# Optimization experiments

Measured on AMD Instinct MI355X. Metric: run time of the kernel, lower is better.

Reference implementation:

```python
import jax, jax.numpy as jnp
import numpy as np

B, S, D_MODEL = 8, 2048, 512
G, V = 2, 320          # num_groups, num_vars
CV_DIM = 256 // G      # proj_dim // num_groups = 128
TAU = 2.0


def setup_inputs() -> dict:
    key = jax.random.key(0)
    k1, k2, k3, k4, k5 = jax.random.split(key, 5)
    hidden_states = jax.random.normal(k1, (B, S, D_MODEL), dtype=jnp.float32)
    # Linear(d_model -> G*V); store as (in, out) for direct matmul
    W = jax.random.normal(k2, (D_MODEL, G * V), dtype=jnp.float32) * (1.0 / np.sqrt(D_MODEL))
    b = jax.random.normal(k3, (G * V,), dtype=jnp.float32) * 0.01
    codevectors = jax.random.normal(k4, (1, G * V, CV_DIM), dtype=jnp.float32)
    # pre-sampled Gumbel(0,1) noise, shape (B*S*G, V)
    u = jax.random.uniform(k5, (B * S * G, V), dtype=jnp.float32,
                           minval=1e-10, maxval=1.0)
    gumbels = -jnp.log(-jnp.log(u))
    return {"hidden_states": hidden_states, "W": W, "b": b,
            "codevectors": codevectors, "gumbels": gumbels}


def reference(hidden_states, W, b, codevectors, gumbels):
    Bs, Ss, _ = hidden_states.shape
    N = Bs * Ss
    # weight projection: (B,S,D) @ (D,G*V) -> (B,S,G*V)
    logits = hidden_states @ W + b
    logits = logits.reshape(N * G, V).astype(jnp.float32)

    # gumbel-softmax, hard=True with straight-through
    y_soft = jax.nn.softmax((logits + gumbels) / TAU, axis=-1)  # (N*G, V)
    idx = jnp.argmax(y_soft, axis=-1)
    y_hard = jax.nn.one_hot(idx, V, dtype=y_soft.dtype)
    codevector_probs = y_hard - jax.lax.stop_gradient(y_soft) + y_soft

    # perplexity from the (noise-free) soft distribution
    soft_dist = jax.nn.softmax(logits.reshape(N, G, V), axis=-1)
    marginal = soft_dist.mean(axis=0)                            # (G, V)
    perplexity = jnp.exp(-jnp.sum(marginal * jnp.log(marginal + 1e-7),
                                  axis=-1)).sum()

    # codebook lookup as weighted sum (equivalent to one-hot gather)
    cv = codevectors.reshape(G, V, CV_DIM)
    probs = codevector_probs.reshape(N, G, V)
    out = jnp.einsum('ngv,gvd->ngd', probs, cv)                  # (N, G, d)
    out = out.reshape(Bs, Ss, G * CV_DIM)
    return out, perplexity
```

## Files before the change

kernel.cpp:

```cpp
#include <hip/hip_runtime.h>

#define M_ROWS 16384
#define K_DIM  512
#define N_COLS 640
#define V_CODES 320
#define CV_DIM 128

typedef _Float16 half8 __attribute__((ext_vector_type(8)));
typedef _Float16 half4v __attribute__((ext_vector_type(4)));
typedef float floatx4 __attribute__((ext_vector_type(4)));

__device__ inline void gll16(const void* g, void* l) {
    __builtin_amdgcn_global_load_lds(
        (const __attribute__((address_space(1))) void*)g,
        (__attribute__((address_space(3))) void*)l, 16, 0, 0);
}

__global__ __launch_bounds__(256)
void prepW(const float* __restrict__ W, _Float16* __restrict__ Wt,
           float* __restrict__ marginal) {
    __shared__ float tile[32][33];
    const int b = blockIdx.x, t = threadIdx.x;
    if (b == 320) {
        for (int i = t; i < 640; i += 256) marginal[i] = 0.f;
        return;
    }
    const int n0 = (b % 20) * 32, k0 = (b / 20) * 32;
    {
        const int kk = t >> 3, nn4 = (t & 7) << 2;
        const float4 w = *(const float4*)(W + (size_t)(k0 + kk) * 640 + n0 + nn4);
        tile[kk][nn4 + 0] = w.x; tile[kk][nn4 + 1] = w.y;
        tile[kk][nn4 + 2] = w.z; tile[kk][nn4 + 3] = w.w;
    }
    __syncthreads();
    {
        const int nn = t >> 3, kk4 = (t & 7) << 2;
        half4v h = {(_Float16)tile[kk4 + 0][nn], (_Float16)tile[kk4 + 1][nn],
                    (_Float16)tile[kk4 + 2][nn], (_Float16)tile[kk4 + 3][nn]};
        *(half4v*)(Wt + (size_t)(n0 + nn) * 512 + k0 + kk4) = h;
    }
}

__global__ __launch_bounds__(512, 2)
void fused(const float* __restrict__ A, const _Float16* __restrict__ Bt,
           const float* __restrict__ bias, const float* __restrict__ gum,
           const float* __restrict__ cv, float* __restrict__ out,
           float* __restrict__ marginal) {
    __shared__ _Float16 As[2][64 * 32];
    __shared__ _Float16 Bs[2][640 * 32];
    __shared__ float smarg[640];
    const int t = threadIdx.x;
    const int wave = t >> 6, lane = t & 63;
    const int bm = blockIdx.x;
    const int mi = wave >> 1, g = wave & 1;
    const int c = lane & 15, kq = lane >> 4;

    for (int i = t; i < 640; i += 512) smarg[i] = 0.f;

    floatx4 acc[20];
#pragma unroll
    for (int nt = 0; nt < 20; ++nt) acc[nt] = (floatx4){0.f, 0.f, 0.f, 0.f};

    const int am = t >> 3, ad = t & 7;
    const int a_wr = am * 64 + (((ad >> 1) ^ (am & 3)) << 4) + (ad & 1) * 8;
    const float* Aptr = A + (size_t)(bm * 64 + am) * 512 + ad * 4;

    auto STAGE = [&](int buf, int k0) {
        const float4 av = *(const float4*)(Aptr + k0);
#pragma unroll
        for (int s = 0; s < 5; ++s) {
            const int qq = t + 512 * s;
            const int n  = qq >> 2, j = qq & 3;
            gll16(Bt + (size_t)n * 512 + k0 + ((j ^ (n & 3)) << 3),
                  (char*)(&Bs[buf][0]) + qq * 16);
        }
        const half4v h = {(_Float16)av.x, (_Float16)av.y,
                          (_Float16)av.z, (_Float16)av.w};
        *(half4v*)((char*)(&As[buf][0]) + a_wr) = h;
    };

    STAGE(0, 0);
    __syncthreads();

    for (int kt = 0; kt < 16; ++kt) {
        const int cur = kt & 1;
        if (kt < 15) STAGE(cur ^ 1, (kt + 1) * 32);
        const int ra = mi * 16 + c;
        const half8 af = *(const half8*)((const char*)(&As[cur][0]) +
                          ra * 64 + ((kq ^ (ra & 3)) << 4));
#pragma unroll
        for (int nt = 0; nt < 20; ++nt) {
            const int rb = g * 320 + nt * 16 + c;
            const half8 bf = *(const half8*)((const char*)(&Bs[cur][0]) +
                              rb * 64 + ((kq ^ (rb & 3)) << 4));
            acc[nt] = __builtin_amdgcn_mfma_f32_16x16x32_f16(af, bf, acc[nt], 0, 0, 0);
        }
        __syncthreads();
    }

    float bcol[20];
#pragma unroll
    for (int nt = 0; nt < 20; ++nt) bcol[nt] = bias[g * 320 + nt * 16 + c];

    float mcontrib[20];
#pragma unroll
    for (int nt = 0; nt < 20; ++nt) mcontrib[nt] = 0.f;

#pragma unroll
    for (int rg = 0; rg < 4; ++rg) {
        const int ntok = bm * 64 + mi * 16 + kq * 4 + rg;
        float lg[20];
#pragma unroll
        for (int nt = 0; nt < 20; ++nt) lg[nt] = acc[nt][rg] + bcol[nt];
        const float* gr = gum + ((size_t)ntok * 2 + g) * V_CODES + c;
        float gv[20];
#pragma unroll
        for (int nt = 0; nt < 20; ++nt) gv[nt] = gr[nt * 16];
        float best = -1e30f; int bidx = 0;
#pragma unroll
        for (int nt = 0; nt < 20; ++nt) {
            const float nz = lg[nt] + gv[nt];
            const int v = nt * 16 + c;
            if (nz > best) { best = nz; bidx = v; }
        }
#pragma unroll
        for (int mask = 1; mask <= 8; mask <<= 1) {
            const float ob = __shfl_xor(best, mask);
            const int   oi = __shfl_xor(bidx, mask);
            if (ob > best || (ob == best && oi < bidx)) { best = ob; bidx = oi; }
        }
        float s = 0.f;
#pragma unroll
        for (int nt = 0; nt < 20; ++nt) { lg[nt] = __expf(lg[nt]); s += lg[nt]; }
#pragma unroll
        for (int mask = 1; mask <= 8; mask <<= 1) s += __shfl_xor(s, mask);
        const float inv = 1.f / s;
#pragma unroll
        for (int nt = 0; nt < 20; ++nt) mcontrib[nt] += lg[nt] * inv;
        const float4* cvp = (const float4*)(cv + ((size_t)g * V_CODES + bidx) * CV_DIM)
                            + c * 2;
        const float4 v0 = cvp[0], v1 = cvp[1];
        float4* op = (float4*)(out + (size_t)ntok * 256 + g * CV_DIM) + c * 2;
        op[0] = v0; op[1] = v1;
    }

#pragma unroll
    for (int nt = 0; nt < 20; ++nt) {
        mcontrib[nt] += __shfl_xor(mcontrib[nt], 16);
        mcontrib[nt] += __shfl_xor(mcontrib[nt], 32);
    }
    if (lane < 16) {
#pragma unroll
        for (int nt = 0; nt < 20; ++nt)
            atomicAdd(&smarg[g * V_CODES + nt * 16 + c], mcontrib[nt]);
    }
    __syncthreads();
    for (int i = t; i < 640; i += 512) atomicAdd(marginal + i, smarg[i]);
}

__global__ __launch_bounds__(640)
void finalize(const float* __restrict__ marginal, float* __restrict__ perp_out) {
    __shared__ float terms[640];
    __shared__ float gsum[2];
    const int t = threadIdx.x;

    const float m = marginal[t] * (1.0f / (float)M_ROWS);
    terms[t] = -m * __logf(m + 1e-7f);
    __syncthreads();

    if (t < 128) {
        const int g = t >> 6, lane = t & 63;
        float e = 0.f;
#pragma unroll
        for (int j = 0; j < 5; ++j) e += terms[g * V_CODES + lane + 64 * j];
#pragma unroll
        for (int off = 32; off; off >>= 1) e += __shfl_down(e, off);
        if (lane == 0) gsum[g] = e;
    }
    __syncthreads();
    if (t == 0) perp_out[0] = __expf(gsum[0]) + __expf(gsum[1]);
}

extern "C" void kernel_launch(void* const* d_in, const int* in_sizes, int n_in,
                              void* d_out, int out_size, void* d_ws, size_t ws_size,
                              hipStream_t stream) {
    (void)in_sizes; (void)n_in; (void)out_size; (void)ws_size;
    const float* hs = (const float*)d_in[0];
    const float* W  = (const float*)d_in[1];
    const float* bi = (const float*)d_in[2];
    const float* cv = (const float*)d_in[3];
    const float* gu = (const float*)d_in[4];
    float* out = (float*)d_out;

    _Float16* Wt       = (_Float16*)d_ws;
    float*    marginal = (float*)(Wt + (size_t)N_COLS * K_DIM);

    prepW<<<321, 256, 0, stream>>>(W, Wt, marginal);
    fused<<<256, 512, 0, stream>>>(hs, Wt, bi, gu, cv, out, marginal);
    finalize<<<1, 640, 0, stream>>>(marginal, out + (size_t)M_ROWS * 256);
}
```

Baseline: 54.06 us.

## Split fused GEMM blocks by codebook group into a 2D grid

Each fused block now handles one of the two codebook groups, launched over a (256,2) grid with 256 threads instead of one 512-thread block covering both groups. The block stages only its group's 320 columns of the fp16 weight, so the B tile in shared memory is half the size, and A loads widen to 8 elements per thread. This doubles the number of blocks and should improve occupancy and CU coverage, at the cost of each A tile being loaded and converted twice, once per group.

```diff
diff --git a/kernel.cpp b/kernel.cpp
--- a/kernel.cpp
+++ b/kernel.cpp
@@ -41,42 +41,46 @@
     }
 }
 
-__global__ __launch_bounds__(512, 2)
+__global__ __launch_bounds__(256, 2)
 void fused(const float* __restrict__ A, const _Float16* __restrict__ Bt,
            const float* __restrict__ bias, const float* __restrict__ gum,
            const float* __restrict__ cv, float* __restrict__ out,
            float* __restrict__ marginal) {
     __shared__ _Float16 As[2][64 * 32];
-    __shared__ _Float16 Bs[2][640 * 32];
-    __shared__ float smarg[640];
+    __shared__ _Float16 Bs[2][320 * 32];
+    __shared__ float smarg[320];
     const int t = threadIdx.x;
     const int wave = t >> 6, lane = t & 63;
-    const int bm = blockIdx.x;
-    const int mi = wave >> 1, g = wave & 1;
+    const int bm = blockIdx.x, g = blockIdx.y;
+    const int mi = wave;
     const int c = lane & 15, kq = lane >> 4;
 
-    for (int i = t; i < 640; i += 512) smarg[i] = 0.f;
+    for (int i = t; i < 320; i += 256) smarg[i] = 0.f;
 
     floatx4 acc[20];
 #pragma unroll
     for (int nt = 0; nt < 20; ++nt) acc[nt] = (floatx4){0.f, 0.f, 0.f, 0.f};
 
-    const int am = t >> 3, ad = t & 7;
-    const int a_wr = am * 64 + (((ad >> 1) ^ (am & 3)) << 4) + (ad & 1) * 8;
-    const float* Aptr = A + (size_t)(bm * 64 + am) * 512 + ad * 4;
+    const int am = t >> 2, ad = t & 3;
+    const int a_wr = am * 64 + ((ad ^ (am & 3)) << 4);
+    const float* Aptr = A + (size_t)(bm * 64 + am) * 512 + ad * 8;
+
+    const _Float16* Bg = Bt + (size_t)g * V_CODES * K_DIM;
 
     auto STAGE = [&](int buf, int k0) {
-        const float4 av = *(const float4*)(Aptr + k0);
+        const float4 av0 = *(const float4*)(Aptr + k0);
+        const float4 av1 = *(const float4*)(Aptr + k0 + 4);
 #pragma unroll
         for (int s = 0; s < 5; ++s) {
-            const int qq = t + 512 * s;
-            const int n  = qq >> 2, j = qq & 3;
-            gll16(Bt + (size_t)n * 512 + k0 + ((j ^ (n & 3)) << 3),
-                  (char*)(&Bs[buf][0]) + qq * 16);
-        }
-        const half4v h = {(_Float16)av.x, (_Float16)av.y,
-                          (_Float16)av.z, (_Float16)av.w};
-        *(half4v*)((char*)(&As[buf][0]) + a_wr) = h;
+            const int q = t + 256 * s;
+            const int n = q >> 2, j = q & 3;
+            gll16(Bg + (size_t)n * 512 + k0 + ((j ^ (n & 3)) << 3),
+                  (char*)(&Bs[buf][0]) + q * 16);
+        }
+        const half8 h = {(_Float16)av0.x, (_Float16)av0.y, (_Float16)av0.z,
+                         (_Float16)av0.w, (_Float16)av1.x, (_Float16)av1.y,
+                         (_Float16)av1.z, (_Float16)av1.w};
+        *(half8*)((char*)(&As[buf][0]) + a_wr) = h;
     };
 
     STAGE(0, 0);
@@ -90,7 +94,7 @@
                           ra * 64 + ((kq ^ (ra & 3)) << 4));
 #pragma unroll
         for (int nt = 0; nt < 20; ++nt) {
-            const int rb = g * 320 + nt * 16 + c;
+            const int rb = nt * 16 + c;
             const half8 bf = *(const half8*)((const char*)(&Bs[cur][0]) +
                               rb * 64 + ((kq ^ (rb & 3)) << 4));
             acc[nt] = __builtin_amdgcn_mfma_f32_16x16x32_f16(af, bf, acc[nt], 0, 0, 0);
@@ -100,7 +104,7 @@
 
     float bcol[20];
 #pragma unroll
-    for (int nt = 0; nt < 20; ++nt) bcol[nt] = bias[g * 320 + nt * 16 + c];
+    for (int nt = 0; nt < 20; ++nt) bcol[nt] = bias[g * V_CODES + nt * 16 + c];
 
     float mcontrib[20];
 #pragma unroll
@@ -152,10 +156,11 @@
     if (lane < 16) {
 #pragma unroll
         for (int nt = 0; nt < 20; ++nt)
-            atomicAdd(&smarg[g * V_CODES + nt * 16 + c], mcontrib[nt]);
-    }
-    __syncthreads();
-    for (int i = t; i < 640; i += 512) atomicAdd(marginal + i, smarg[i]);
+            atomicAdd(&smarg[nt * 16 + c], mcontrib[nt]);
+    }
+    __syncthreads();
+    for (int i = t; i < 320; i += 256)
+        atomicAdd(marginal + g * V_CODES + i, smarg[i]);
 }
 
 __global__ __launch_bounds__(640)
@@ -196,6 +201,6 @@
     float*    marginal = (float*)(Wt + (size_t)N_COLS * K_DIM);
 
     prepW<<<321, 256, 0, stream>>>(W, Wt, marginal);
-    fused<<<256, 512, 0, stream>>>(hs, Wt, bi, gu, cv, out, marginal);
+    fused<<<dim3(256, 2), 256, 0, stream>>>(hs, Wt, bi, gu, cv, out, marginal);
     finalize<<<1, 640, 0, stream>>>(marginal, out + (size_t)M_ROWS * 256);
 }
```

Measured after the change: 49.01 us. 1.1x faster.
